# Kernel tuning notes

Hardware: AMD Instinct MI355X
Metric: run time of the kernel (lower is better)

## Reference

```python
import jax, jax.numpy as jnp
import numpy as np

C = 64
G = 4          # group_number
K = 3          # kernel_size
R = 4          # reduction_ratio -> bottleneck C//R = 16
BN_EPS = 1e-3  # keras BatchNormalization default epsilon


def setup_inputs() -> dict:
    key = jax.random.key(0)
    ks = jax.random.split(key, 8)
    B, H, W = 8, 192, 192
    cr = C // R
    x = jax.random.normal(ks[0], (B, H, W, C), dtype=jnp.float32)
    # kernel_gen: Conv2D 1x1 (C -> C//R), BN, ReLU, Conv2D 1x1 (C//R -> K*K*G)
    w1 = jax.random.normal(ks[1], (C, cr), dtype=jnp.float32) * (1.0 / np.sqrt(C))
    b1 = jnp.zeros((cr,), dtype=jnp.float32)
    gamma = 1.0 + 0.1 * jax.random.normal(ks[2], (cr,), dtype=jnp.float32)
    beta = 0.1 * jax.random.normal(ks[3], (cr,), dtype=jnp.float32)
    mean = 0.1 * jax.random.normal(ks[4], (cr,), dtype=jnp.float32)
    var = jax.random.uniform(ks[5], (cr,), dtype=jnp.float32, minval=0.5, maxval=1.5)
    w2 = jax.random.normal(ks[6], (cr, K * K * G), dtype=jnp.float32) * (1.0 / np.sqrt(cr))
    b2 = jnp.zeros((K * K * G,), dtype=jnp.float32)
    return {"x": x, "w1": w1, "b1": b1, "gamma": gamma, "beta": beta,
            "mean": mean, "var": var, "w2": w2, "b2": b2}


def reference(x, w1, b1, gamma, beta, mean, var, w2, b2):
    B, H, W, Cc = x.shape
    # --- kernel generation (stride=1 -> identity pooling) ---
    t = jnp.einsum('bhwc,cd->bhwd', x, w1) + b1                 # [B,H,W,C//R]
    t = (t - mean) * jax.lax.rsqrt(var + BN_EPS) * gamma + beta  # BN (inference)
    t = jax.nn.relu(t)
    kern = jnp.einsum('bhwd,de->bhwe', t, w2) + b2               # [B,H,W,K*K*G]
    kern = kern.reshape(B, H, W, K * K, 1, G)
    # --- unfold: tf.image.extract_patches SAME, stride 1, patch order (ki,kj,C) ---
    pad = K // 2
    xp = jnp.pad(x, ((0, 0), (pad, pad), (pad, pad), (0, 0)))
    patches = jnp.stack(
        [xp[:, i:i + H, j:j + W, :] for i in range(K) for j in range(K)],
        axis=3)                                                  # [B,H,W,K*K,C]
    unfolded = patches.reshape(B, H, W, K * K, Cc // G, G)
    # --- per-pixel multiply-reduce over patch axis ---
    out = jnp.sum(kern * unfolded, axis=3)                       # [B,H,W,C//G,G]
    return out.reshape(B, H, W, Cc)
```

## Files before the change

kernel.cpp:

```cpp
#include <hip/hip_runtime.h>


#define B_   8
#define H_   192
#define W_   192
#define CR_  16
#define TH_  8
#define TW_  16
#define TILES_X (W_/TW_)
#define TILES_PER_IMG (TILES_X*(H_/TH_))
#define NBLK (B_*TILES_PER_IMG)
#define NPIX (TH_*TW_)

constexpr float BN_EPS = 1e-3f;

template <bool INTERIOR>
__device__ __forceinline__ void tap_load(const float* __restrict__ ximg,
                                         int h, int w, int c4i,
                                         float4 (&xv)[9], int& m9)
{
    m9 = 0x1FF;
    #pragma unroll
    for (int ti = 0; ti < 3; ++ti) {
        int hh = h + ti - 1;
        bool vh = true;
        if (!INTERIOR) {
            vh = (unsigned)hh < (unsigned)H_;
            hh = hh < 0 ? 0 : (hh >= H_ ? H_ - 1 : hh);
        }
        #pragma unroll
        for (int tj = 0; tj < 3; ++tj) {
            int ww = w + tj - 1;
            if (!INTERIOR) {
                const bool v = vh && ((unsigned)ww < (unsigned)W_);
                ww = ww < 0 ? 0 : (ww >= W_ ? W_ - 1 : ww);
                if (!v) m9 &= ~(1 << (ti * 3 + tj));
            }
            xv[ti * 3 + tj] = reinterpret_cast<const float4*>(
                ximg + (((size_t)(hh * W_ + ww)) << 6))[c4i];
        }
    }
}

template <bool INTERIOR>
__device__ __forceinline__ void phase_b(const float* __restrict__ x,
                                        float* __restrict__ out,
                                        const float4* __restrict__ s_kern,
                                        int img, int th0, int tw0, int tid)
{
    const int prow = tid >> 4;
    const int c4i  = tid & 15;
    const float* ximg = x + (((size_t)(img * H_ * W_)) << 6);
    float* oimg = out + (((size_t)(img * H_ * W_)) << 6);

    auto hw_of = [&](int i, int& h, int& w, int& q) {
        q = i * 8 + prow;
        h = th0 + (q >> 4);
        w = tw0 + (q & 15);
    };

    float4 xa[9]; int ma;
    {
        int h, w, q;
        hw_of(0, h, w, q);
        tap_load<INTERIOR>(ximg, h, w, c4i, xa, ma);
    }

    for (int i = 0; i < 16; ++i) {
        float4 xb[9]; int mb = 0x1FF;
        if (i + 1 < 16) {
            int hn, wn, qn;
            hw_of(i + 1, hn, wn, qn);
            tap_load<INTERIOR>(ximg, hn, wn, c4i, xb, mb);
        }

        int h, w, q;
        hw_of(i, h, w, q);
        const float4* kq = &s_kern[q * 9];

        float4 acc = make_float4(0.f, 0.f, 0.f, 0.f);
        #pragma unroll
        for (int t = 0; t < 9; ++t) {
            float4 kv = kq[t];
            if (!INTERIOR) {
                const bool v = (ma >> t) & 1;
                kv.x = v ? kv.x : 0.f;
                kv.y = v ? kv.y : 0.f;
                kv.z = v ? kv.z : 0.f;
                kv.w = v ? kv.w : 0.f;
            }
            acc.x = fmaf(kv.x, xa[t].x, acc.x);
            acc.y = fmaf(kv.y, xa[t].y, acc.y);
            acc.z = fmaf(kv.z, xa[t].z, acc.z);
            acc.w = fmaf(kv.w, xa[t].w, acc.w);
        }
        reinterpret_cast<float4*>(oimg + (((size_t)(h * W_ + w)) << 6))[c4i] = acc;

        #pragma unroll
        for (int t = 0; t < 9; ++t) xa[t] = xb[t];
        ma = mb;
    }
}

__global__ __launch_bounds__(128, 4)
void invol_fused(const float* __restrict__ x,
                 const float* __restrict__ w1,
                 const float* __restrict__ b1,
                 const float* __restrict__ gamma,
                 const float* __restrict__ beta,
                 const float* __restrict__ mean,
                 const float* __restrict__ var,
                 const float* __restrict__ w2,
                 const float* __restrict__ b2,
                 float* __restrict__ out)
{
    __shared__ float4 s_kern[NPIX * 9];

    const int bid = blockIdx.x;
    const int img = bid & 7;
    const int tin = bid >> 3;
    const int th0 = (tin / TILES_X) * TH_;
    const int tw0 = (tin % TILES_X) * TW_;

    const int tid = threadIdx.x;

    {
        const int r = tid >> 4, cc = tid & 15;
        const int h = th0 + r, w = tw0 + cc;
        const float4* xp = reinterpret_cast<const float4*>(
            x + (((size_t)((img * H_ + h) * W_ + w)) << 6));

        float td[CR_];
        #pragma unroll
        for (int d = 0; d < CR_; ++d) td[d] = 0.f;

        #pragma unroll
        for (int c4 = 0; c4 < 16; ++c4) {
            const float4 xv = xp[c4];
            const float xs[4] = {xv.x, xv.y, xv.z, xv.w};
            #pragma unroll
            for (int k = 0; k < 4; ++k) {
                const float* wr = w1 + (c4 * 4 + k) * CR_;
                #pragma unroll
                for (int d = 0; d < CR_; ++d)
                    td[d] = fmaf(xs[k], wr[d], td[d]);
            }
        }

        #pragma unroll
        for (int d = 0; d < CR_; ++d) {
            const float a = gamma[d] * rsqrtf(var[d] + BN_EPS);
            const float c = (b1[d] - mean[d]) * a + beta[d];
            td[d] = fmaxf(fmaf(td[d], a, c), 0.f);
        }

        float ke[36];
        #pragma unroll
        for (int e = 0; e < 36; ++e) ke[e] = b2[e];
        #pragma unroll
        for (int d = 0; d < CR_; ++d) {
            const float t = td[d];
            const float* wr = w2 + d * 36;
            #pragma unroll
            for (int e = 0; e < 36; ++e)
                ke[e] = fmaf(t, wr[e], ke[e]);
        }

        float4* skq = &s_kern[tid * 9];
        #pragma unroll
        for (int t9 = 0; t9 < 9; ++t9)
            skq[t9] = make_float4(ke[t9 * 4 + 0], ke[t9 * 4 + 1],
                                  ke[t9 * 4 + 2], ke[t9 * 4 + 3]);
    }

    __syncthreads();

    const bool interior = (th0 > 0) && (th0 + TH_ < H_) &&
                          (tw0 > 0) && (tw0 + TW_ < W_);
    if (interior)
        phase_b<true>(x, out, s_kern, img, th0, tw0, tid);
    else
        phase_b<false>(x, out, s_kern, img, th0, tw0, tid);
}

extern "C" void kernel_launch(void* const* d_in, const int* in_sizes, int n_in,
                              void* d_out, int out_size, void* d_ws, size_t ws_size,
                              hipStream_t stream) {
    const float* x     = (const float*)d_in[0];
    const float* w1    = (const float*)d_in[1];
    const float* b1    = (const float*)d_in[2];
    const float* gamma = (const float*)d_in[3];
    const float* beta  = (const float*)d_in[4];
    const float* mean  = (const float*)d_in[5];
    const float* var   = (const float*)d_in[6];
    const float* w2    = (const float*)d_in[7];
    const float* b2    = (const float*)d_in[8];
    float* out = (float*)d_out;

    invol_fused<<<dim3(NBLK), dim3(128), 0, stream>>>(
        x, w1, b1, gamma, beta, mean, var, w2, b2, out);
}
```

Measured before the change: 198.9 us.

## Split fused involution into separate kernel-gen and apply kernels via workspace

When the workspace is large enough, the fused kernel is replaced by two launches. The first computes the per-pixel 36-tap dynamic kernels and writes them to global memory. The second applies them with one thread per pixel and 4-channel group, using a swizzled block index across images. This removes the shared-memory tile and the __syncthreads barrier between the two phases and gives the apply step more parallelism, at the cost of an extra global write and read of about 42 MB of kernel weights. The fallback fused path also drops its software prefetch of the next pixel's taps.

```diff
diff --git a/kernel.cpp b/kernel.cpp
--- a/kernel.cpp
+++ b/kernel.cpp
@@ -5,135 +5,192 @@
 #define H_   192
 #define W_   192
 #define CR_  16
+#define NPX  (B_*H_*W_)
+#define KWS  ((size_t)NPX * 36 * 4)
+
+constexpr float BN_EPS = 1e-3f;
+
+__global__ __launch_bounds__(256)
+void kern_gen(const float* __restrict__ x,
+              const float* __restrict__ w1,
+              const float* __restrict__ b1,
+              const float* __restrict__ gamma,
+              const float* __restrict__ beta,
+              const float* __restrict__ mean,
+              const float* __restrict__ var,
+              const float* __restrict__ w2,
+              const float* __restrict__ b2,
+              float* __restrict__ kern)
+{
+    const int bid = blockIdx.x;
+    const int img = bid & 7;
+    const int px_in_img = (bid >> 3) * 256 + threadIdx.x;
+    const int px = img * (H_ * W_) + px_in_img;
+
+    const float4* xp = reinterpret_cast<const float4*>(x + ((size_t)px << 6));
+
+    float td[CR_];
+    #pragma unroll
+    for (int d = 0; d < CR_; ++d) td[d] = 0.f;
+
+    #pragma unroll
+    for (int c4 = 0; c4 < 16; ++c4) {
+        const float4 xv = xp[c4];
+        const float xs[4] = {xv.x, xv.y, xv.z, xv.w};
+        #pragma unroll
+        for (int k = 0; k < 4; ++k) {
+            const float* wr = w1 + (c4 * 4 + k) * CR_;
+            #pragma unroll
+            for (int d = 0; d < CR_; ++d)
+                td[d] = fmaf(xs[k], wr[d], td[d]);
+        }
+    }
+
+    #pragma unroll
+    for (int d = 0; d < CR_; ++d) {
+        const float a = gamma[d] * rsqrtf(var[d] + BN_EPS);
+        const float c = (b1[d] - mean[d]) * a + beta[d];
+        td[d] = fmaxf(fmaf(td[d], a, c), 0.f);
+    }
+
+    float ke[36];
+    #pragma unroll
+    for (int e = 0; e < 36; ++e) ke[e] = b2[e];
+    #pragma unroll
+    for (int d = 0; d < CR_; ++d) {
+        const float t = td[d];
+        const float* wr = w2 + d * 36;
+        #pragma unroll
+        for (int e = 0; e < 36; ++e)
+            ke[e] = fmaf(t, wr[e], ke[e]);
+    }
+
+    float4* kq = reinterpret_cast<float4*>(kern + (size_t)px * 36);
+    #pragma unroll
+    for (int t = 0; t < 9; ++t)
+        kq[t] = make_float4(ke[4 * t], ke[4 * t + 1], ke[4 * t + 2], ke[4 * t + 3]);
+}
+
+__global__ __launch_bounds__(256)
+void invol_apply(const float* __restrict__ x,
+                 const float* __restrict__ kern,
+                 float* __restrict__ out)
+{
+    const int bid = blockIdx.x;
+    const int bsw = (bid & 7) * 2304 + (bid >> 3);
+    const int task = bsw * 256 + threadIdx.x;
+    const int px  = task >> 4;
+    const int c4i = task & 15;
+
+    const int img = px / (H_ * W_);
+    const int rem = px - img * (H_ * W_);
+    const int h = rem / W_;
+    const int w = rem - h * W_;
+
+    const float* ximg = x + (((size_t)(img * H_ * W_)) << 6);
+
+    float4 xv[9];
+    int m9 = 0;
+    #pragma unroll
+    for (int ti = 0; ti < 3; ++ti) {
+        int hh = h + ti - 1;
+        const bool vh = (unsigned)hh < (unsigned)H_;
+        hh = hh < 0 ? 0 : (hh >= H_ ? H_ - 1 : hh);
+        #pragma unroll
+        for (int tj = 0; tj < 3; ++tj) {
+            int ww = w + tj - 1;
+            const bool v = vh && ((unsigned)ww < (unsigned)W_);
+            ww = ww < 0 ? 0 : (ww >= W_ ? W_ - 1 : ww);
+            if (v) m9 |= 1 << (ti * 3 + tj);
+            xv[ti * 3 + tj] = reinterpret_cast<const float4*>(
+                ximg + (((size_t)(hh * W_ + ww)) << 6))[c4i];
+        }
+    }
+
+    const float4* kq = reinterpret_cast<const float4*>(kern + (size_t)px * 36);
+    float4 acc = make_float4(0.f, 0.f, 0.f, 0.f);
+    #pragma unroll
+    for (int t = 0; t < 9; ++t) {
+        const bool v = (m9 >> t) & 1;
+        const float4 kv = kq[t];
+        const float kx = v ? kv.x : 0.f;
+        const float ky = v ? kv.y : 0.f;
+        const float kz = v ? kv.z : 0.f;
+        const float kw = v ? kv.w : 0.f;
+        acc.x = fmaf(kx, xv[t].x, acc.x);
+        acc.y = fmaf(ky, xv[t].y, acc.y);
+        acc.z = fmaf(kz, xv[t].z, acc.z);
+        acc.w = fmaf(kw, xv[t].w, acc.w);
+    }
+    reinterpret_cast<float4*>(out)[task] = acc;
+}
+
 #define TH_  8
 #define TW_  16
 #define TILES_X (W_/TW_)
-#define TILES_PER_IMG (TILES_X*(H_/TH_))
-#define NBLK (B_*TILES_PER_IMG)
 #define NPIX (TH_*TW_)
 
-constexpr float BN_EPS = 1e-3f;
-
 template <bool INTERIOR>
-__device__ __forceinline__ void tap_load(const float* __restrict__ ximg,
-                                         int h, int w, int c4i,
-                                         float4 (&xv)[9], int& m9)
-{
-    m9 = 0x1FF;
-    #pragma unroll
-    for (int ti = 0; ti < 3; ++ti) {
-        int hh = h + ti - 1;
-        bool vh = true;
-        if (!INTERIOR) {
-            vh = (unsigned)hh < (unsigned)H_;
-            hh = hh < 0 ? 0 : (hh >= H_ ? H_ - 1 : hh);
-        }
-        #pragma unroll
-        for (int tj = 0; tj < 3; ++tj) {
-            int ww = w + tj - 1;
-            if (!INTERIOR) {
-                const bool v = vh && ((unsigned)ww < (unsigned)W_);
-                ww = ww < 0 ? 0 : (ww >= W_ ? W_ - 1 : ww);
-                if (!v) m9 &= ~(1 << (ti * 3 + tj));
-            }
-            xv[ti * 3 + tj] = reinterpret_cast<const float4*>(
-                ximg + (((size_t)(hh * W_ + ww)) << 6))[c4i];
-        }
-    }
-}
-
-template <bool INTERIOR>
-__device__ __forceinline__ void phase_b(const float* __restrict__ x,
-                                        float* __restrict__ out,
-                                        const float4* __restrict__ s_kern,
-                                        int img, int th0, int tw0, int tid)
+__device__ __forceinline__ void phase_b_f(const float* __restrict__ x,
+                                          float* __restrict__ out,
+                                          const float4* __restrict__ s_kern,
+                                          int img, int th0, int tw0, int tid)
 {
     const int prow = tid >> 4;
     const int c4i  = tid & 15;
     const float* ximg = x + (((size_t)(img * H_ * W_)) << 6);
     float* oimg = out + (((size_t)(img * H_ * W_)) << 6);
 
-    auto hw_of = [&](int i, int& h, int& w, int& q) {
-        q = i * 8 + prow;
-        h = th0 + (q >> 4);
-        w = tw0 + (q & 15);
-    };
-
-    float4 xa[9]; int ma;
-    {
-        int h, w, q;
-        hw_of(0, h, w, q);
-        tap_load<INTERIOR>(ximg, h, w, c4i, xa, ma);
-    }
-
     for (int i = 0; i < 16; ++i) {
-        float4 xb[9]; int mb = 0x1FF;
-        if (i + 1 < 16) {
-            int hn, wn, qn;
-            hw_of(i + 1, hn, wn, qn);
-            tap_load<INTERIOR>(ximg, hn, wn, c4i, xb, mb);
-        }
-
-        int h, w, q;
-        hw_of(i, h, w, q);
+        const int q = i * 8 + prow;
+        const int h = th0 + (q >> 4), w = tw0 + (q & 15);
         const float4* kq = &s_kern[q * 9];
-
         float4 acc = make_float4(0.f, 0.f, 0.f, 0.f);
         #pragma unroll
-        for (int t = 0; t < 9; ++t) {
-            float4 kv = kq[t];
-            if (!INTERIOR) {
-                const bool v = (ma >> t) & 1;
-                kv.x = v ? kv.x : 0.f;
-                kv.y = v ? kv.y : 0.f;
-                kv.z = v ? kv.z : 0.f;
-                kv.w = v ? kv.w : 0.f;
+        for (int ti = 0; ti < 3; ++ti) {
+            int hh = h + ti - 1;
+            bool vh = true;
+            if (!INTERIOR) { vh = (unsigned)hh < (unsigned)H_; hh = hh < 0 ? 0 : (hh >= H_ ? H_-1 : hh); }
+            #pragma unroll
+            for (int tj = 0; tj < 3; ++tj) {
+                int ww = w + tj - 1;
+                bool v = vh;
+                if (!INTERIOR) { v = vh && ((unsigned)ww < (unsigned)W_); ww = ww < 0 ? 0 : (ww >= W_-1 ? W_-1 : ww); }
+                const float4 xvv = reinterpret_cast<const float4*>(
+                    ximg + (((size_t)(hh * W_ + ww)) << 6))[c4i];
+                float4 kv = kq[ti * 3 + tj];
+                if (!INTERIOR) { kv.x = v?kv.x:0.f; kv.y = v?kv.y:0.f; kv.z = v?kv.z:0.f; kv.w = v?kv.w:0.f; }
+                acc.x = fmaf(kv.x, xvv.x, acc.x);
+                acc.y = fmaf(kv.y, xvv.y, acc.y);
+                acc.z = fmaf(kv.z, xvv.z, acc.z);
+                acc.w = fmaf(kv.w, xvv.w, acc.w);
             }
-            acc.x = fmaf(kv.x, xa[t].x, acc.x);
-            acc.y = fmaf(kv.y, xa[t].y, acc.y);
-            acc.z = fmaf(kv.z, xa[t].z, acc.z);
-            acc.w = fmaf(kv.w, xa[t].w, acc.w);
         }
         reinterpret_cast<float4*>(oimg + (((size_t)(h * W_ + w)) << 6))[c4i] = acc;
-
-        #pragma unroll
-        for (int t = 0; t < 9; ++t) xa[t] = xb[t];
-        ma = mb;
     }
 }
 
 __global__ __launch_bounds__(128, 4)
-void invol_fused(const float* __restrict__ x,
-                 const float* __restrict__ w1,
-                 const float* __restrict__ b1,
-                 const float* __restrict__ gamma,
-                 const float* __restrict__ beta,
-                 const float* __restrict__ mean,
-                 const float* __restrict__ var,
-                 const float* __restrict__ w2,
-                 const float* __restrict__ b2,
-                 float* __restrict__ out)
+void invol_fused(const float* __restrict__ x, const float* __restrict__ w1,
+                 const float* __restrict__ b1, const float* __restrict__ gamma,
+                 const float* __restrict__ beta, const float* __restrict__ mean,
+                 const float* __restrict__ var, const float* __restrict__ w2,
+                 const float* __restrict__ b2, float* __restrict__ out)
 {
     __shared__ float4 s_kern[NPIX * 9];
-
     const int bid = blockIdx.x;
     const int img = bid & 7;
     const int tin = bid >> 3;
     const int th0 = (tin / TILES_X) * TH_;
     const int tw0 = (tin % TILES_X) * TW_;
-
     const int tid = threadIdx.x;
-
     {
-        const int r = tid >> 4, cc = tid & 15;
-        const int h = th0 + r, w = tw0 + cc;
+        const int h = th0 + (tid >> 4), w = tw0 + (tid & 15);
         const float4* xp = reinterpret_cast<const float4*>(
             x + (((size_t)((img * H_ + h) * W_ + w)) << 6));
-
         float td[CR_];
         #pragma unroll
         for (int d = 0; d < CR_; ++d) td[d] = 0.f;
-
         #pragma unroll
         for (int c4 = 0; c4 < 16; ++c4) {
             const float4 xv = xp[c4];
@@ -142,18 +199,15 @@
             for (int k = 0; k < 4; ++k) {
                 const float* wr = w1 + (c4 * 4 + k) * CR_;
                 #pragma unroll
-                for (int d = 0; d < CR_; ++d)
-                    td[d] = fmaf(xs[k], wr[d], td[d]);
+                for (int d = 0; d < CR_; ++d) td[d] = fmaf(xs[k], wr[d], td[d]);
             }
         }
-
         #pragma unroll
         for (int d = 0; d < CR_; ++d) {
             const float a = gamma[d] * rsqrtf(var[d] + BN_EPS);
             const float c = (b1[d] - mean[d]) * a + beta[d];
             td[d] = fmaxf(fmaf(td[d], a, c), 0.f);
         }
-
         float ke[36];
         #pragma unroll
         for (int e = 0; e < 36; ++e) ke[e] = b2[e];
@@ -162,25 +216,18 @@
             const float t = td[d];
             const float* wr = w2 + d * 36;
             #pragma unroll
-            for (int e = 0; e < 36; ++e)
-                ke[e] = fmaf(t, wr[e], ke[e]);
-        }
-
+            for (int e = 0; e < 36; ++e) ke[e] = fmaf(t, wr[e], ke[e]);
+        }
         float4* skq = &s_kern[tid * 9];
         #pragma unroll
         for (int t9 = 0; t9 < 9; ++t9)
-            skq[t9] = make_float4(ke[t9 * 4 + 0], ke[t9 * 4 + 1],
-                                  ke[t9 * 4 + 2], ke[t9 * 4 + 3]);
-    }
-
+            skq[t9] = make_float4(ke[4*t9], ke[4*t9+1], ke[4*t9+2], ke[4*t9+3]);
+    }
     __syncthreads();
-
     const bool interior = (th0 > 0) && (th0 + TH_ < H_) &&
                           (tw0 > 0) && (tw0 + TW_ < W_);
-    if (interior)
-        phase_b<true>(x, out, s_kern, img, th0, tw0, tid);
-    else
-        phase_b<false>(x, out, s_kern, img, th0, tw0, tid);
+    if (interior) phase_b_f<true>(x, out, s_kern, img, th0, tw0, tid);
+    else          phase_b_f<false>(x, out, s_kern, img, th0, tw0, tid);
 }
 
 extern "C" void kernel_launch(void* const* d_in, const int* in_sizes, int n_in,
@@ -197,6 +244,14 @@
     const float* b2    = (const float*)d_in[8];
     float* out = (float*)d_out;
 
-    invol_fused<<<dim3(NBLK), dim3(128), 0, stream>>>(
-        x, w1, b1, gamma, beta, mean, var, w2, b2, out);
-}
+    if (ws_size >= KWS) {
+        float* kern = (float*)d_ws;
+        kern_gen<<<dim3(NPX / 256), dim3(256), 0, stream>>>(
+            x, w1, b1, gamma, beta, mean, var, w2, b2, kern);
+        invol_apply<<<dim3(NPX * 16 / 256), dim3(256), 0, stream>>>(
+            x, kern, out);
+    } else {
+        invol_fused<<<dim3(NPX / NPIX), dim3(128), 0, stream>>>(
+            x, w1, b1, gamma, beta, mean, var, w2, b2, out);
+    }
+}
```

New measurement: 203.6 us. +2.3%, slower.
